# Kernel optimization log

Hardware: AMD Instinct MI355X
Metric: run time of the kernel (lower is better)

## Reference

```python
import jax, jax.numpy as jnp
import numpy as np

H, W = 1024, 2048      # dims from __init__
C = 34                 # Cityscapes label ids 0..33 (thing classes 24..33)
N_INST = 128           # instance capacity (len(instance_probs))


def setup_inputs() -> dict:
    key = jax.random.key(0)
    k1, k2, k3, k4 = jax.random.split(key, 4)
    return {
        "segmentation_map": jax.random.randint(k1, (H, W), 0, C, dtype=jnp.int32),
        "instance_maps": jax.random.randint(k2, (H, W), 0, N_INST + 1, dtype=jnp.int32),
        "seg_map_probs": jax.random.uniform(k3, (C, H, W), dtype=jnp.float32),
        "instance_probs": jax.random.uniform(k4, (N_INST,), dtype=jnp.float32),
    }


def reference(segmentation_map, instance_maps, seg_map_probs, instance_probs):
    # nn.Threshold(23.99, 50): x if x > 23.99 else 50; then things = (thresh <= 33)
    seg_f = segmentation_map.astype(jnp.float32)
    things = (seg_f > 23.99) & (seg_f <= 33.0)           # (H, W) bool
    inst = jnp.where(things, instance_maps, 0)            # zero-out non-thing pixels

    flat_inst = inst.reshape(-1)                          # (HW,)
    flat_seg = segmentation_map.reshape(-1)               # (HW,)

    # segmented histogram: pixel counts per (instance, class)
    pair_idx = flat_inst * C + flat_seg
    counts2d = jax.ops.segment_sum(
        jnp.ones_like(flat_inst), pair_idx, num_segments=(N_INST + 1) * C
    ).reshape(N_INST + 1, C)

    # segmented sum of every class prob map over each instance mask
    probs_pix = seg_map_probs.reshape(C, -1).T            # (HW, C)
    sums2d = jax.ops.segment_sum(probs_pix, flat_inst, num_segments=N_INST + 1)  # (N+1, C)

    counts = counts2d[1:]                                 # drop background id 0 -> (N, C)
    sums = sums2d[1:]                                     # (N, C)

    inst_class = jnp.argmax(counts, axis=1).astype(jnp.int32)     # mode class per instance
    total = counts.sum(axis=1)                                     # seg_counts.sum()
    # mean of the winning class's prob map over the instance mask
    seg_prob = jnp.take_along_axis(sums, inst_class[:, None], axis=1)[:, 0] / jnp.maximum(
        total, 1
    ).astype(seg_map_probs.dtype)

    # per-instance binary masks, uint8 like the torch code
    inst_ids = jnp.arange(1, N_INST + 1, dtype=inst.dtype)
    inst_masks = (inst[None, :, :] == inst_ids[:, None, None]).astype(jnp.uint8)  # (N, H, W)

    valid = total > 0   # which instance slots actually appear in the image
    return inst_masks, inst_class, instance_probs, seg_prob, total, valid
```

## Files before the change

### kernel.cpp

```cpp
#include <hip/hip_runtime.h>

#define HH   1024
#define WW   2048
#define HWP  (HH * WW)
#define CC   34
#define NI   128
#define THING_LO 24
#define THING_HI 33
#define NTC  10

typedef float nfloat4 __attribute__((ext_vector_type(4)));

#define OFF_CLASS  ((size_t)NI * HWP)
#define OFF_PROBS  (OFF_CLASS + NI)
#define OFF_SEGP   (OFF_PROBS + NI)
#define OFF_TOTAL  (OFF_SEGP + NI)
#define OFF_VALID  (OFF_TOTAL + NI)

#define WS_COUNTS  0
#define WS_CLS     (NI * NTC * 4)
#define WS_INV     (WS_CLS + NI * 4)

__device__ __forceinline__ int thing_inst(int s, int im) {
    return (s >= THING_LO && s <= THING_HI) ? im : 0;
}

__global__ __launch_bounds__(256) void k1_mask_count(
    const int* __restrict__ seg, const int* __restrict__ imap,
    float* __restrict__ out_masks, int* __restrict__ counts)
{
    const int t = blockIdx.x * 256 + threadIdx.x;
    const int p = t * 4;
    const int4 sg = *reinterpret_cast<const int4*>(seg + p);
    const int4 im = *reinterpret_cast<const int4*>(imap + p);

    const int i0 = thing_inst(sg.x, im.x);
    const int i1 = thing_inst(sg.y, im.y);
    const int i2 = thing_inst(sg.z, im.z);
    const int i3 = thing_inst(sg.w, im.w);

    if (i0 > 0) atomicAdd(&counts[(i0 - 1) * NTC + (sg.x - THING_LO)], 1);
    if (i1 > 0) atomicAdd(&counts[(i1 - 1) * NTC + (sg.y - THING_LO)], 1);
    if (i2 > 0) atomicAdd(&counts[(i2 - 1) * NTC + (sg.z - THING_LO)], 1);
    if (i3 > 0) atomicAdd(&counts[(i3 - 1) * NTC + (sg.w - THING_LO)], 1);

    float* o = out_masks + p;
    #pragma unroll
    for (int i = 1; i <= NI; ++i) {
        nfloat4 v;
        v.x = (i0 == i) ? 1.0f : 0.0f;
        v.y = (i1 == i) ? 1.0f : 0.0f;
        v.z = (i2 == i) ? 1.0f : 0.0f;
        v.w = (i3 == i) ? 1.0f : 0.0f;
        *reinterpret_cast<nfloat4*>(o) = v;
        o += HWP;
    }
}

__global__ __launch_bounds__(128) void k2_stats(
    const int* __restrict__ counts, const float* __restrict__ iprobs,
    float* __restrict__ out, int* __restrict__ cls_ws, float* __restrict__ inv_ws)
{
    const int i = threadIdx.x;
    int bestv = 0, bestc = 0, tot = 0;
    #pragma unroll
    for (int j = 0; j < NTC; ++j) {
        const int c = counts[i * NTC + j];
        tot += c;
        if (c > bestv) { bestv = c; bestc = THING_LO + j; }
    }
    cls_ws[i] = bestc;
    inv_ws[i] = 1.0f / (float)(tot > 0 ? tot : 1);
    out[OFF_CLASS + i] = (float)bestc;
    out[OFF_PROBS + i] = iprobs[i];
    out[OFF_SEGP  + i] = 0.0f;
    out[OFF_TOTAL + i] = (float)tot;
    out[OFF_VALID + i] = (tot > 0) ? 1.0f : 0.0f;
}

__global__ __launch_bounds__(256) void k3_segsum(
    const int* __restrict__ seg, const int* __restrict__ imap,
    const float* __restrict__ probs, const int* __restrict__ cls_ws,
    const float* __restrict__ inv_ws, float* __restrict__ out)
{
    __shared__ float lsum[NI];
    __shared__ int   scls[NI];
    if (threadIdx.x < NI) {
        lsum[threadIdx.x] = 0.0f;
        scls[threadIdx.x] = cls_ws[threadIdx.x];
    }
    __syncthreads();

    const int stride = gridDim.x * blockDim.x;
    for (int t = blockIdx.x * blockDim.x + threadIdx.x; t < HWP / 4; t += stride) {
        const int p = t * 4;
        const int4 sg = *reinterpret_cast<const int4*>(seg + p);
        const int4 im = *reinterpret_cast<const int4*>(imap + p);
        const int ii[4] = { thing_inst(sg.x, im.x), thing_inst(sg.y, im.y),
                            thing_inst(sg.z, im.z), thing_inst(sg.w, im.w) };
        #pragma unroll
        for (int k = 0; k < 4; ++k) {
            if (ii[k] > 0) {
                const int inst = ii[k] - 1;
                const size_t idx = (size_t)scls[inst] * HWP + (size_t)(p + k);
                atomicAdd(&lsum[inst], probs[idx]);
            }
        }
    }
    __syncthreads();
    if (threadIdx.x < NI) {
        const float v = lsum[threadIdx.x];
        if (v != 0.0f)
            atomicAdd(&out[OFF_SEGP + threadIdx.x], v * inv_ws[threadIdx.x]);
    }
}

extern "C" void kernel_launch(void* const* d_in, const int* in_sizes, int n_in,
                              void* d_out, int out_size, void* d_ws, size_t ws_size,
                              hipStream_t stream) {
    const int*   seg    = (const int*)d_in[0];
    const int*   imap   = (const int*)d_in[1];
    const float* probs  = (const float*)d_in[2];
    const float* iprobs = (const float*)d_in[3];
    float* out = (float*)d_out;

    char* ws = (char*)d_ws;
    int*   counts = (int*)(ws + WS_COUNTS);
    int*   cls_ws = (int*)(ws + WS_CLS);
    float* inv_ws = (float*)(ws + WS_INV);

    (void)hipMemsetAsync(counts, 0, NI * NTC * sizeof(int), stream);

    k1_mask_count<<<(HWP / 4) / 256, 256, 0, stream>>>(seg, imap, out, counts);
    k2_stats<<<1, 128, 0, stream>>>(counts, iprobs, out, cls_ws, inv_ws);
    k3_segsum<<<256, 256, 0, stream>>>(seg, imap, probs, cls_ws, inv_ws, out);
}
```

Baseline: 1.283 ms.

## Privatize class histogram in LDS and tile mask writes per chunk

The mask/count kernel now gives each block an 8192-pixel chunk. Per-instance class counts are accumulated in a shared-memory histogram and flushed to global memory with one atomic per nonzero bin, instead of one global atomic per thing pixel. Instance ids are packed four per word in LDS, and each wavefront writes 32 instance planes over the whole chunk. The segsum kernel's grid grows from 256 to 1024 blocks. This cuts global atomic contention, but the output stays dominated by the roughly 1 GB float mask write, and the flush adds up to 1280 atomics per block.

```diff
diff --git a/kernel.cpp b/kernel.cpp
--- a/kernel.cpp
+++ b/kernel.cpp
@@ -8,6 +8,9 @@
 #define THING_LO 24
 #define THING_HI 33
 #define NTC  10
+
+#define CHUNK 8192
+#define QPB   (CHUNK / 4)
 
 typedef float nfloat4 __attribute__((ext_vector_type(4)));
 
@@ -29,31 +32,59 @@
     const int* __restrict__ seg, const int* __restrict__ imap,
     float* __restrict__ out_masks, int* __restrict__ counts)
 {
-    const int t = blockIdx.x * 256 + threadIdx.x;
-    const int p = t * 4;
-    const int4 sg = *reinterpret_cast<const int4*>(seg + p);
-    const int4 im = *reinterpret_cast<const int4*>(imap + p);
+    __shared__ uint32_t inst4[QPB];
+    __shared__ int      hist[NI * NTC];
 
-    const int i0 = thing_inst(sg.x, im.x);
-    const int i1 = thing_inst(sg.y, im.y);
-    const int i2 = thing_inst(sg.z, im.z);
-    const int i3 = thing_inst(sg.w, im.w);
+    const int tid = threadIdx.x;
 
-    if (i0 > 0) atomicAdd(&counts[(i0 - 1) * NTC + (sg.x - THING_LO)], 1);
-    if (i1 > 0) atomicAdd(&counts[(i1 - 1) * NTC + (sg.y - THING_LO)], 1);
-    if (i2 > 0) atomicAdd(&counts[(i2 - 1) * NTC + (sg.z - THING_LO)], 1);
-    if (i3 > 0) atomicAdd(&counts[(i3 - 1) * NTC + (sg.w - THING_LO)], 1);
+    for (int i = tid; i < NI * NTC; i += 256) hist[i] = 0;
+    __syncthreads();
 
-    float* o = out_masks + p;
+    const int base_q = blockIdx.x * QPB;
     #pragma unroll
-    for (int i = 1; i <= NI; ++i) {
-        nfloat4 v;
-        v.x = (i0 == i) ? 1.0f : 0.0f;
-        v.y = (i1 == i) ? 1.0f : 0.0f;
-        v.z = (i2 == i) ? 1.0f : 0.0f;
-        v.w = (i3 == i) ? 1.0f : 0.0f;
-        *reinterpret_cast<nfloat4*>(o) = v;
-        o += HWP;
+    for (int j = 0; j < QPB / 256; ++j) {
+        const int q = base_q + j * 256 + tid;
+        const int p = q * 4;
+        const int4 sg = *reinterpret_cast<const int4*>(seg + p);
+        const int4 im = *reinterpret_cast<const int4*>(imap + p);
+
+        const int i0 = thing_inst(sg.x, im.x);
+        const int i1 = thing_inst(sg.y, im.y);
+        const int i2 = thing_inst(sg.z, im.z);
+        const int i3 = thing_inst(sg.w, im.w);
+
+        if (i0 > 0) atomicAdd(&hist[(i0 - 1) * NTC + (sg.x - THING_LO)], 1);
+        if (i1 > 0) atomicAdd(&hist[(i1 - 1) * NTC + (sg.y - THING_LO)], 1);
+        if (i2 > 0) atomicAdd(&hist[(i2 - 1) * NTC + (sg.z - THING_LO)], 1);
+        if (i3 > 0) atomicAdd(&hist[(i3 - 1) * NTC + (sg.w - THING_LO)], 1);
+
+        inst4[j * 256 + tid] = (uint32_t)i0 | ((uint32_t)i1 << 8) |
+                               ((uint32_t)i2 << 16) | ((uint32_t)i3 << 24);
+    }
+    __syncthreads();
+
+    for (int i = tid; i < NI * NTC; i += 256) {
+        const int v = hist[i];
+        if (v) atomicAdd(&counts[i], v);
+    }
+
+    const int w = tid >> 6;
+    const int l = tid & 63;
+    float* obase = out_masks + (size_t)blockIdx.x * CHUNK + (size_t)(l * 4);
+
+    for (int ip = 0; ip < 32; ++ip) {
+        const uint32_t id = (uint32_t)(w * 32 + ip + 1);
+        float* o = obase + (size_t)(w * 32 + ip) * HWP;
+        #pragma unroll 8
+        for (int s = 0; s < 32; ++s) {
+            const uint32_t qq = inst4[s * 64 + l];
+            nfloat4 v;
+            v.x = ((qq & 0xffu)         == id) ? 1.0f : 0.0f;
+            v.y = (((qq >> 8)  & 0xffu) == id) ? 1.0f : 0.0f;
+            v.z = (((qq >> 16) & 0xffu) == id) ? 1.0f : 0.0f;
+            v.w = ((qq >> 24)           == id) ? 1.0f : 0.0f;
+            *reinterpret_cast<nfloat4*>(o + s * 256) = v;
+        }
     }
 }
 
@@ -131,7 +162,7 @@
 
     (void)hipMemsetAsync(counts, 0, NI * NTC * sizeof(int), stream);
 
-    k1_mask_count<<<(HWP / 4) / 256, 256, 0, stream>>>(seg, imap, out, counts);
+    k1_mask_count<<<HWP / CHUNK, 256, 0, stream>>>(seg, imap, out, counts);
     k2_stats<<<1, 128, 0, stream>>>(counts, iprobs, out, cls_ws, inv_ws);
-    k3_segsum<<<256, 256, 0, stream>>>(seg, imap, probs, cls_ws, inv_ws, out);
+    k3_segsum<<<1024, 256, 0, stream>>>(seg, imap, probs, cls_ws, inv_ws, out);
 }
```

Result: faster. 1.213 ms (-5.5%).
